# Performance work log

Hardware: AMD Instinct MI355X
Metric: run time of the kernel (lower is better)

Reference implementation:

```python
import jax, jax.numpy as jnp
import numpy as np

IMG_H = IMG_W = 640
NUM_CLASSES = 80
B = 8
NUM_ANCHORS = 76725
MAX_TOTAL = 200          # max_total_size == max_size_per_class
SCORE_TH = 0.5
IOU_TH = 0.5
K_CAND = 256             # per-class candidate pool for NMS (>= max survivors)
VARIANCES = jnp.asarray([0.1, 0.1, 0.2, 0.2], jnp.float32)


def _build_anchors(img_h, img_w):
    # RetinaNet AnchorBox: levels 3..7, 3 ratios x 3 scales, [cx, cy, w, h]
    ratios = [0.5, 1.0, 2.0]
    scales = [2.0 ** x for x in (0.0, 1.0 / 3.0, 2.0 / 3.0)]
    areas = [s * s for s in (32.0, 64.0, 128.0, 256.0, 512.0)]
    out = []
    for lvl, stride in enumerate([2 ** i for i in range(3, 8)]):
        dims = []
        for r in ratios:
            h = np.sqrt(areas[lvl] / r)
            w = areas[lvl] / h
            for s in scales:
                dims.append([w * s, h * s])
        dims = np.asarray(dims, np.float32)                      # [9,2]
        fh = int(np.ceil(img_h / stride)); fw = int(np.ceil(img_w / stride))
        rx = (np.arange(fw, dtype=np.float32) + 0.5) * stride
        ry = (np.arange(fh, dtype=np.float32) + 0.5) * stride
        cx, cy = np.meshgrid(rx, ry)
        centers = np.broadcast_to(np.stack([cx, cy], -1)[:, :, None, :], (fh, fw, 9, 2))
        d = np.broadcast_to(dims[None, None], (fh, fw, 9, 2))
        out.append(np.concatenate([centers, d], -1).reshape(-1, 4))
    return jnp.asarray(np.concatenate(out, 0))                   # [A,4]


def setup_inputs() -> dict:
    key = jax.random.key(0)
    k1, k2 = jax.random.split(key)
    box_pred = jax.random.normal(k1, (B, NUM_ANCHORS, 4), jnp.float32)
    cls_pred = jax.random.normal(k2, (B, NUM_ANCHORS, NUM_CLASSES), jnp.float32)
    anchor_boxes = _build_anchors(IMG_H, IMG_W)
    return {"box_pred": box_pred, "cls_pred": cls_pred, "anchor_boxes": anchor_boxes}


def _iou_one_vs_many(box, boxes):
    # box [4] vs boxes [K,4] in corner format
    lt = jnp.maximum(box[:2], boxes[:, :2])
    rb = jnp.minimum(box[2:], boxes[:, 2:])
    wh = jnp.maximum(rb - lt, 0.0)
    inter = wh[:, 0] * wh[:, 1]
    a1 = (box[2] - box[0]) * (box[3] - box[1])
    a2 = (boxes[:, 2] - boxes[:, 0]) * (boxes[:, 3] - boxes[:, 1])
    return inter / jnp.maximum(a1 + a2 - inter, 1e-8)


def _nms_keep(boxes, scores):
    # boxes [K,4] already sorted by descending score; greedy NMS
    eligible = scores > SCORE_TH
    idx = jnp.arange(K_CAND)

    def body(i, keep):
        iou = _iou_one_vs_many(boxes[i], boxes)
        suppress = (iou > IOU_TH) & (idx > i)
        return jnp.where(keep[i], keep & ~suppress, keep)

    keep = jax.lax.fori_loop(0, K_CAND, body, eligible)
    keep = keep & ((jnp.cumsum(keep) - 1) < MAX_TOTAL)           # max_size_per_class cap
    return keep


def _decode_and_nms(box_pred, cls_pred, anchor_boxes):
    scores_all = jax.nn.sigmoid(cls_pred)                        # [B,A,C]
    # decode: (dx,dy,dw,dh)*variances against [cx,cy,w,h] anchors
    d = box_pred * VARIANCES
    xy = d[..., :2] * anchor_boxes[None, :, 2:] + anchor_boxes[None, :, :2]
    wh = jnp.exp(d[..., 2:]) * anchor_boxes[None, :, 2:]
    boxes = jnp.concatenate([xy - 0.5 * wh, xy + 0.5 * wh], -1)  # [B,A,4] corners

    sc = jnp.swapaxes(scores_all, 1, 2)                          # [B,C,A]
    top_sc, top_idx = jax.lax.top_k(sc, K_CAND)                  # [B,C,K] sorted desc
    cand_boxes = jnp.take_along_axis(boxes[:, None], top_idx[..., None], axis=2)  # [B,C,K,4]

    keep = jax.lax.stop_gradient(jax.vmap(jax.vmap(_nms_keep))(cand_boxes, top_sc))  # [B,C,K]
    sel = jnp.where(keep, top_sc, -1.0)

    flat_sc = sel.reshape(B, -1)                                 # [B,C*K]
    flat_boxes = cand_boxes.reshape(B, -1, 4)
    flat_lbl = jnp.broadcast_to(jnp.arange(NUM_CLASSES)[None, :, None],
                                (B, NUM_CLASSES, K_CAND)).reshape(B, -1)

    fs, fi = jax.lax.top_k(flat_sc, MAX_TOTAL)                   # combine across classes
    out_boxes = jnp.take_along_axis(flat_boxes, fi[..., None], axis=1)
    out_lbl = jnp.take_along_axis(flat_lbl, fi, axis=1).astype(jnp.float32)
    valid = fs > 0.0                                             # pad invalid slots
    return (jnp.where(valid[..., None], out_boxes, 0.0),
            jnp.where(valid, fs, 0.0),
            jnp.where(valid, out_lbl, -1.0))


def reference(box_pred, cls_pred, anchor_boxes):
    return _decode_and_nms(box_pred, cls_pred, anchor_boxes)
```

## Files before the change

kernel.cpp:

```cpp
#include <hip/hip_runtime.h>
#include <math.h>
#include <stdint.h>

typedef unsigned long long u64;
typedef unsigned int u32;

#define NB 8
#define NA 76725
#define NC 80
#define KC 256
#define MAXT 200
#define CAP 2048
#define SORTN 512
#define TAU 2.0f
#define CHUNK 512
#define NCHUNK 150
#define BCAP 48
#define CSTRIDE 16

#define OFF_BUFA      0ull
#define OFF_CLASSLIST 10485760ull
#define OFF_CANDBOX   11796480ull
#define OFF_COUNTS    14417920ull

__device__ __forceinline__ void kf_proc(float4 v, int i, int a0,
                                        u64 (*bucket)[BCAP], u32* bcnt) {
  int a = a0 + i / (NC / 4);
  int c0 = (i % (NC / 4)) * 4;
  float vv[4] = {v.x, v.y, v.z, v.w};
#pragma unroll
  for (int j = 0; j < 4; j++) {
    if (vv[j] > TAU) {
      int c = c0 + j;
      u32 pos = atomicAdd(&bcnt[c], 1u);
      if (pos < BCAP)
        bucket[c][pos] = ((u64)__float_as_uint(vv[j]) << 32) | (u32)a;
    }
  }
}

__global__ __launch_bounds__(256) void kfilter(const float* __restrict__ cls,
                                               u64* __restrict__ bufA,
                                               u32* __restrict__ counts) {
  __shared__ u64 bucket[NC][BCAP];
  __shared__ u32 bcnt[NC];
  __shared__ u32 gbase[NC];
  __shared__ u32 pref[NC + 1];

  const int b = blockIdx.x / NCHUNK;
  const int ch = blockIdx.x % NCHUNK;
  const int tid = threadIdx.x;
  const int a0 = ch * CHUNK;
  const int aN = (NA - a0) < CHUNK ? (NA - a0) : CHUNK;

  for (int i = tid; i < NC; i += 256) bcnt[i] = 0;
  __syncthreads();

  const float4* p = (const float4*)(cls + ((size_t)b * NA + a0) * NC);
  const int n4 = aN * (NC / 4);
  for (int i0 = tid; i0 < n4; i0 += 1024) {
    float4 v0, v1, v2, v3;
    const bool g1 = i0 + 256 < n4, g2 = i0 + 512 < n4, g3 = i0 + 768 < n4;
    v0 = p[i0];
    if (g1) v1 = p[i0 + 256];
    if (g2) v2 = p[i0 + 512];
    if (g3) v3 = p[i0 + 768];
    kf_proc(v0, i0, a0, bucket, bcnt);
    if (g1) kf_proc(v1, i0 + 256, a0, bucket, bcnt);
    if (g2) kf_proc(v2, i0 + 512, a0, bucket, bcnt);
    if (g3) kf_proc(v3, i0 + 768, a0, bucket, bcnt);
  }
  __syncthreads();
  if (tid < NC) {
    u32 n = bcnt[tid];
    if (n > BCAP) n = BCAP;
    bcnt[tid] = n;
    gbase[tid] = atomicAdd(&counts[(b * NC + tid) * CSTRIDE], n);
  }
  __syncthreads();
  if (tid == 0) {
    u32 s = 0;
    for (int c = 0; c < NC; c++) { pref[c] = s; s += bcnt[c]; }
    pref[NC] = s;
  }
  __syncthreads();
  const int total = (int)pref[NC];
  for (int e = tid; e < total; e += 256) {
    int lo = 0, hi = NC;
    while (lo + 1 < hi) { int mid = (lo + hi) >> 1; if ((int)pref[mid] <= e) lo = mid; else hi = mid; }
    int c = lo;
    int loc = e - (int)pref[c];
    u32 gb = gbase[c] + (u32)loc;
    if (gb < CAP)
      bufA[((size_t)(b * NC + c)) * CAP + gb] = bucket[c][loc];
  }
}

__global__ __launch_bounds__(256) void kselect(
    const float* __restrict__ cls, const float* __restrict__ boxp,
    const float* __restrict__ anc, u64* __restrict__ bufA,
    const u32* __restrict__ counts, u64* __restrict__ classList,
    float4* __restrict__ candBox) {
  __shared__ u64 sbuf[CAP];
  __shared__ u32 hist[1024];
  __shared__ int sbsum[64];
  __shared__ int sT, sNsel, sExtra;
  __shared__ u64 skey[SORTN];
  __shared__ float4 sBox[KC];
  __shared__ float sAr[KC];

  const int tid = threadIdx.x;
  const int bc = blockIdx.x;
  const int b = bc / NC, c = bc % NC;
  u64* buf = bufA + (size_t)bc * CAP;

  int cnt0 = (int)counts[bc * CSTRIDE];
  if (cnt0 > CAP) cnt0 = CAP;
  int cnt = cnt0;
  if (cnt0 < KC) {
    if (tid == 0) sExtra = 0;
    __syncthreads();
    for (int a = tid; a < NA; a += 256) {
      float x = cls[((size_t)b * NA + a) * NC + c];
      if (x > 0.0f && !(x > TAU)) {
        int pos = cnt0 + atomicAdd(&sExtra, 1);
        if (pos < CAP) buf[pos] = ((u64)__float_as_uint(x) << 32) | (u32)a;
      }
    }
    __syncthreads();
    cnt = cnt0 + sExtra;
  }
  if (cnt > CAP) cnt = CAP;

  for (int i = tid; i < 1024; i += 256) hist[i] = 0;
  if (tid == 0) sNsel = 0;
  for (int e = tid; e < cnt; e += 256) sbuf[e] = buf[e];
  __syncthreads();

  for (int e = tid; e < cnt; e += 256) {
    float f = __uint_as_float((u32)(sbuf[e] >> 32));
    int bin = (int)(f * 170.0f);
    bin = bin < 0 ? 0 : (bin > 1023 ? 1023 : bin);
    atomicAdd(&hist[bin], 1u);
  }
  __syncthreads();
  if (tid < 64) {
    int s = 0;
    for (int i = 0; i < 16; i++) s += (int)hist[tid * 16 + i];
    sbsum[tid] = s;
  }
  __syncthreads();
  if (tid == 0) {
    int acc = 0, sb = 63;
    while (sb >= 0 && acc + sbsum[sb] < KC) { acc += sbsum[sb]; sb--; }
    int T = 0;
    if (sb >= 0) {
      int bin = sb * 16 + 15;
      while (bin > sb * 16 && acc + (int)hist[bin] < KC) {
        acc += (int)hist[bin];
        bin--;
      }
      T = bin;
    }
    sT = T;
  }
  __syncthreads();
  const int T = sT;

  for (int e = tid; e < cnt; e += 256) {
    u64 k = sbuf[e];
    float f = __uint_as_float((u32)(k >> 32));
    int bin = (int)(f * 170.0f);
    bin = bin < 0 ? 0 : (bin > 1023 ? 1023 : bin);
    if (bin >= T) {
      float sc = 1.0f / (1.0f + expf(-f));
      u32 a = (u32)k;
      int pos = atomicAdd(&sNsel, 1);
      if (pos < SORTN)
        skey[pos] = ((u64)__float_as_uint(sc) << 32) | (0xFFFFFFFFu - a);
    }
  }
  __syncthreads();
  int nsel = sNsel;
  if (nsel > SORTN) nsel = SORTN;
  for (int i = tid; i < SORTN; i += 256)
    if (i >= nsel) skey[i] = 0;
  __syncthreads();

  for (int k = 2; k <= SORTN; k <<= 1) {
    for (int j = k >> 1; j > 0; j >>= 1) {
      int i = ((tid & ~(j - 1)) << 1) | (tid & (j - 1));
      int ixj = i | j;
      u64 x = skey[i], y = skey[ixj];
      bool desc = ((i & k) == 0);
      if (desc ? (x < y) : (x > y)) { skey[i] = y; skey[ixj] = x; }
      __syncthreads();
    }
  }

  {
    u64 k = skey[tid];
    u32 a = 0xFFFFFFFFu - (u32)k;
    if (k == 0ull || a >= NA) a = 0;
    float4 p = ((const float4*)boxp)[(size_t)b * NA + a];
    float4 an = ((const float4*)anc)[a];
    float dx = __fmul_rn(p.x, 0.1f), dy = __fmul_rn(p.y, 0.1f);
    float dw = __fmul_rn(p.z, 0.2f), dh = __fmul_rn(p.w, 0.2f);
    float cx = __fadd_rn(__fmul_rn(dx, an.z), an.x);
    float cy = __fadd_rn(__fmul_rn(dy, an.w), an.y);
    float w = __fmul_rn(expf(dw), an.z);
    float h = __fmul_rn(expf(dh), an.w);
    float4 bx;
    bx.x = __fsub_rn(cx, __fmul_rn(0.5f, w));
    bx.y = __fsub_rn(cy, __fmul_rn(0.5f, h));
    bx.z = __fadd_rn(cx, __fmul_rn(0.5f, w));
    bx.w = __fadd_rn(cy, __fmul_rn(0.5f, h));
    sBox[tid] = bx;
    sAr[tid] = __fmul_rn(__fsub_rn(bx.z, bx.x), __fsub_rn(bx.w, bx.y));
    candBox[(size_t)bc * KC + tid] = bx;
  }
  __syncthreads();

  if (tid < 64) {
    const int ln = tid;
    float x1[4], y1[4], x2[4], y2[4], ar[4];
    int keep = 0;
#pragma unroll
    for (int s = 0; s < 4; s++) {
      int j = s * 64 + ln;
      float4 bj = sBox[j];
      x1[s] = bj.x; y1[s] = bj.y; x2[s] = bj.z; y2[s] = bj.w;
      ar[s] = sAr[j];
      if (skey[j] != 0ull) keep |= (1 << s);
    }
    for (int i = 0; i < KC; i++) {
      float4 bi = sBox[i];
      float ai = sAr[i];
      int sup = 0;
#pragma unroll
      for (int s = 0; s < 4; s++) {
        int j = s * 64 + ln;
        float lx = fmaxf(bi.x, x1[s]), ly = fmaxf(bi.y, y1[s]);
        float rx = fminf(bi.z, x2[s]), ry = fminf(bi.w, y2[s]);
        float wx = fmaxf(__fsub_rn(rx, lx), 0.0f);
        float wy = fmaxf(__fsub_rn(ry, ly), 0.0f);
        float inter = __fmul_rn(wx, wy);
        float uni = fmaxf(__fsub_rn(__fadd_rn(ai, ar[s]), inter), 1e-8f);
        float iou = __fdiv_rn(inter, uni);
        if (j > i && iou > 0.5f) sup |= (1 << s);
      }
      int ki = __shfl(keep, i & 63, 64);
      if ((ki >> (i >> 6)) & 1) keep &= ~sup;
    }
    u64 m[4];
#pragma unroll
    for (int s = 0; s < 4; s++) m[s] = __ballot((keep >> s) & 1);
    int tot = 0;
#pragma unroll
    for (int s = 0; s < 4; s++) tot += __popcll(m[s]);
    int keptTotal = tot < MAXT ? tot : MAXT;
    u64 lmask = (1ull << ln) - 1ull;
    int base = 0;
#pragma unroll
    for (int s = 0; s < 4; s++) {
      int j = s * 64 + ln;
      int cum = base + (int)__popcll(m[s] & lmask);
      if (((keep >> s) & 1) && cum < MAXT) {
        u64 hi = skey[j] >> 32;
        classList[(size_t)bc * KC + cum] =
            (hi << 32) | (u64)(0xFFFFFFFFu - (u32)(c * KC + j));
      }
      base += (int)__popcll(m[s]);
    }
    for (int t2 = ln; t2 < KC; t2 += 64)
      if (t2 >= keptTotal) classList[(size_t)bc * KC + t2] = 0;
  }
}

__device__ __forceinline__ u64 shfl64(u64 v, int src) {
  int lo = __shfl((int)(u32)v, src, 64);
  int hi = __shfl((int)(v >> 32), src, 64);
  return ((u64)(u32)hi << 32) | (u32)lo;
}
__device__ __forceinline__ u64 shflxor64(u64 v, int mask) {
  int lo = __shfl_xor((int)(u32)v, mask, 64);
  int hi = __shfl_xor((int)(v >> 32), mask, 64);
  return ((u64)(u32)hi << 32) | (u32)lo;
}
#define CSWAP(a, b) { if ((a) < (b)) { u64 _t = (a); (a) = (b); (b) = _t; } }

__device__ __forceinline__ void wave_merge(u64 acc[4], const u64 cur[4], int ln) {
  u64 t0 = shfl64(cur[3], 63 - ln);
  u64 t1 = shfl64(cur[2], 63 - ln);
  u64 t2 = shfl64(cur[1], 63 - ln);
  u64 t3 = shfl64(cur[0], 63 - ln);
  acc[0] = acc[0] > t0 ? acc[0] : t0;
  acc[1] = acc[1] > t1 ? acc[1] : t1;
  acc[2] = acc[2] > t2 ? acc[2] : t2;
  acc[3] = acc[3] > t3 ? acc[3] : t3;
  CSWAP(acc[0], acc[2]); CSWAP(acc[1], acc[3]);
  CSWAP(acc[0], acc[1]); CSWAP(acc[2], acc[3]);
#pragma unroll
  for (int s = 32; s >= 1; s >>= 1) {
#pragma unroll
    for (int k = 0; k < 4; k++) {
      u64 o = shflxor64(acc[k], s);
      u64 mx = acc[k] > o ? acc[k] : o;
      u64 mn = acc[k] < o ? acc[k] : o;
      acc[k] = ((ln & s) == 0) ? mx : mn;
    }
  }
}

__global__ __launch_bounds__(256) void kmerge(const u64* __restrict__ classList,
                                              const float4* __restrict__ candBox,
                                              float* __restrict__ out) {
  __shared__ u64 lds[4 * KC];
  const int tid = threadIdx.x, b = blockIdx.x;
  const int w = tid >> 6, ln = tid & 63;
  const u64* base = classList + ((size_t)b * NC + w * 20) * KC;
  u64 acc[4];
#pragma unroll
  for (int k = 0; k < 4; k++) acc[k] = base[k * 64 + ln];
  for (int m = 1; m < 20; m++) {
    u64 cur[4];
#pragma unroll
    for (int k = 0; k < 4; k++) cur[k] = base[(size_t)m * KC + k * 64 + ln];
    wave_merge(acc, cur, ln);
  }
#pragma unroll
  for (int k = 0; k < 4; k++) lds[w * KC + k * 64 + ln] = acc[k];
  __syncthreads();
  if (w == 0) {
    for (int m = 1; m < 4; m++) {
      u64 cur[4];
#pragma unroll
      for (int k = 0; k < 4; k++) cur[k] = lds[m * KC + k * 64 + ln];
      wave_merge(acc, cur, ln);
    }
#pragma unroll
    for (int k = 0; k < 4; k++) lds[k * 64 + ln] = acc[k];
  }
  __syncthreads();
  if (tid < MAXT) {
    u64 k = lds[tid];
    float4 bx = make_float4(0.f, 0.f, 0.f, 0.f);
    float sc = 0.0f, lb = -1.0f;
    if (k != 0ull) {
      sc = __uint_as_float((u32)(k >> 32));
      u32 flat = 0xFFFFFFFFu - (u32)k;
      int cc = (int)(flat >> 8), kk = (int)(flat & 255u);
      bx = candBox[((size_t)b * NC + cc) * KC + kk];
      lb = (float)cc;
    }
    float* ob = out + ((size_t)b * MAXT + tid) * 4;
    ob[0] = bx.x; ob[1] = bx.y; ob[2] = bx.z; ob[3] = bx.w;
    out[NB * MAXT * 4 + b * MAXT + tid] = sc;
    out[NB * MAXT * 4 + NB * MAXT + b * MAXT + tid] = lb;
  }
}

extern "C" void kernel_launch(void* const* d_in, const int* in_sizes, int n_in,
                              void* d_out, int out_size, void* d_ws,
                              size_t ws_size, hipStream_t stream) {
  const float* boxp = (const float*)d_in[0];
  const float* cls = (const float*)d_in[1];
  const float* anc = (const float*)d_in[2];
  char* ws = (char*)d_ws;
  u64* bufA = (u64*)(ws + OFF_BUFA);
  u64* classList = (u64*)(ws + OFF_CLASSLIST);
  float4* candBox = (float4*)(ws + OFF_CANDBOX);
  u32* counts = (u32*)(ws + OFF_COUNTS);

  hipMemsetAsync(counts, 0, NB * NC * CSTRIDE * sizeof(u32), stream);
  kfilter<<<NB * NCHUNK, 256, 0, stream>>>(cls, bufA, counts);
  kselect<<<NB * NC, 256, 0, stream>>>(cls, boxp, anc, bufA, counts, classList,
                                       candBox);
  kmerge<<<NB, 256, 0, stream>>>(classList, candBox, (float*)d_out);
}
```

Baseline: 410.5 us.

## Replace bitonic sort with rank sort and precompute NMS IoU bitmask matrix

Measured after the change: 390.2 us. 1.05x faster.

```diff
diff --git a/kernel.cpp b/kernel.cpp
--- a/kernel.cpp
+++ b/kernel.cpp
@@ -11,7 +11,7 @@
 #define KC 256
 #define MAXT 200
 #define CAP 2048
-#define SORTN 512
+#define SELCAP 768
 #define TAU 2.0f
 #define CHUNK 512
 #define NCHUNK 150
@@ -58,17 +58,17 @@
 
   const float4* p = (const float4*)(cls + ((size_t)b * NA + a0) * NC);
   const int n4 = aN * (NC / 4);
-  for (int i0 = tid; i0 < n4; i0 += 1024) {
-    float4 v0, v1, v2, v3;
-    const bool g1 = i0 + 256 < n4, g2 = i0 + 512 < n4, g3 = i0 + 768 < n4;
-    v0 = p[i0];
-    if (g1) v1 = p[i0 + 256];
-    if (g2) v2 = p[i0 + 512];
-    if (g3) v3 = p[i0 + 768];
-    kf_proc(v0, i0, a0, bucket, bcnt);
-    if (g1) kf_proc(v1, i0 + 256, a0, bucket, bcnt);
-    if (g2) kf_proc(v2, i0 + 512, a0, bucket, bcnt);
-    if (g3) kf_proc(v3, i0 + 768, a0, bucket, bcnt);
+  for (int i0 = tid; i0 < n4; i0 += 2048) {
+    float4 v[8];
+    bool g[8];
+#pragma unroll
+    for (int u = 0; u < 8; u++) {
+      g[u] = (i0 + u * 256) < n4;
+      if (g[u]) v[u] = p[i0 + u * 256];
+    }
+#pragma unroll
+    for (int u = 0; u < 8; u++)
+      if (g[u]) kf_proc(v[u], i0 + u * 256, a0, bucket, bcnt);
   }
   __syncthreads();
   if (tid < NC) {
@@ -103,11 +103,12 @@
     float4* __restrict__ candBox) {
   __shared__ u64 sbuf[CAP];
   __shared__ u32 hist[1024];
-  __shared__ int sbsum[64];
-  __shared__ int sT, sNsel, sExtra;
-  __shared__ u64 skey[SORTN];
+  __shared__ u64 sel[SELCAP];
+  __shared__ u64 skey[KC];
+  __shared__ u64 scolT[4][KC];
   __shared__ float4 sBox[KC];
   __shared__ float sAr[KC];
+  __shared__ int sNsel, sExtra, sSb;
 
   const int tid = threadIdx.x;
   const int bc = blockIdx.x;
@@ -134,6 +135,7 @@
 
   for (int i = tid; i < 1024; i += 256) hist[i] = 0;
   if (tid == 0) sNsel = 0;
+  skey[tid] = 0;
   for (int e = tid; e < cnt; e += 256) sbuf[e] = buf[e];
   __syncthreads();
 
@@ -144,59 +146,48 @@
     atomicAdd(&hist[bin], 1u);
   }
   __syncthreads();
+
   if (tid < 64) {
     int s = 0;
+#pragma unroll
     for (int i = 0; i < 16; i++) s += (int)hist[tid * 16 + i];
-    sbsum[tid] = s;
-  }
-  __syncthreads();
-  if (tid == 0) {
-    int acc = 0, sb = 63;
-    while (sb >= 0 && acc + sbsum[sb] < KC) { acc += sbsum[sb]; sb--; }
-    int T = 0;
-    if (sb >= 0) {
-      int bin = sb * 16 + 15;
-      while (bin > sb * 16 && acc + (int)hist[bin] < KC) {
-        acc += (int)hist[bin];
-        bin--;
-      }
-      T = bin;
-    }
-    sT = T;
-  }
-  __syncthreads();
-  const int T = sT;
+    int suf = s;
+#pragma unroll
+    for (int d = 1; d < 64; d <<= 1) {
+      int t = __shfl_down(suf, d, 64);
+      if (tid + d < 64) suf += t;
+    }
+    u64 mask = __ballot(suf >= KC);
+    int sb = mask ? (63 - __clzll((long long)mask)) : 0;
+    if (tid == 0) sSb = sb;
+  }
+  __syncthreads();
+  const int sb = sSb;
 
   for (int e = tid; e < cnt; e += 256) {
     u64 k = sbuf[e];
     float f = __uint_as_float((u32)(k >> 32));
     int bin = (int)(f * 170.0f);
     bin = bin < 0 ? 0 : (bin > 1023 ? 1023 : bin);
-    if (bin >= T) {
+    if ((bin >> 4) >= sb) {
       float sc = 1.0f / (1.0f + expf(-f));
       u32 a = (u32)k;
       int pos = atomicAdd(&sNsel, 1);
-      if (pos < SORTN)
-        skey[pos] = ((u64)__float_as_uint(sc) << 32) | (0xFFFFFFFFu - a);
+      if (pos < SELCAP)
+        sel[pos] = ((u64)__float_as_uint(sc) << 32) | (0xFFFFFFFFu - a);
     }
   }
   __syncthreads();
   int nsel = sNsel;
-  if (nsel > SORTN) nsel = SORTN;
-  for (int i = tid; i < SORTN; i += 256)
-    if (i >= nsel) skey[i] = 0;
-  __syncthreads();
-
-  for (int k = 2; k <= SORTN; k <<= 1) {
-    for (int j = k >> 1; j > 0; j >>= 1) {
-      int i = ((tid & ~(j - 1)) << 1) | (tid & (j - 1));
-      int ixj = i | j;
-      u64 x = skey[i], y = skey[ixj];
-      bool desc = ((i & k) == 0);
-      if (desc ? (x < y) : (x > y)) { skey[i] = y; skey[ixj] = x; }
-      __syncthreads();
-    }
-  }
+  if (nsel > SELCAP) nsel = SELCAP;
+
+  for (int e = tid; e < nsel; e += 256) {
+    u64 k = sel[e];
+    int r = 0;
+    for (int q = 0; q < nsel; q++) r += (sel[q] > k) ? 1 : 0;
+    if (r < KC) skey[r] = k;
+  }
+  __syncthreads();
 
   {
     u64 k = skey[tid];
@@ -221,36 +212,50 @@
   }
   __syncthreads();
 
+  {
+    const int j = tid;
+    float4 bj = sBox[j];
+    float aj = sAr[j];
+    u64 cw[4] = {0ull, 0ull, 0ull, 0ull};
+    for (int i = 0; i < j; i++) {
+      float4 bi = sBox[i];
+      float ai = sAr[i];
+      float lx = fmaxf(bi.x, bj.x), ly = fmaxf(bi.y, bj.y);
+      float rx = fminf(bi.z, bj.z), ry = fminf(bi.w, bj.w);
+      float wx = fmaxf(__fsub_rn(rx, lx), 0.0f);
+      float wy = fmaxf(__fsub_rn(ry, ly), 0.0f);
+      float inter = __fmul_rn(wx, wy);
+      float uni = fmaxf(__fsub_rn(__fadd_rn(ai, aj), inter), 1e-8f);
+      float iou = __fdiv_rn(inter, uni);
+      if (iou > 0.5f) cw[i >> 6] |= (1ull << (i & 63));
+    }
+#pragma unroll
+    for (int w = 0; w < 4; w++) scolT[w][j] = cw[w];
+  }
+  __syncthreads();
+
   if (tid < 64) {
     const int ln = tid;
-    float x1[4], y1[4], x2[4], y2[4], ar[4];
+    u64 C[4][4];
+#pragma unroll
+    for (int s = 0; s < 4; s++)
+#pragma unroll
+      for (int w = 0; w < 4; w++) C[s][w] = scolT[w][s * 64 + ln];
     int keep = 0;
 #pragma unroll
-    for (int s = 0; s < 4; s++) {
-      int j = s * 64 + ln;
-      float4 bj = sBox[j];
-      x1[s] = bj.x; y1[s] = bj.y; x2[s] = bj.z; y2[s] = bj.w;
-      ar[s] = sAr[j];
-      if (skey[j] != 0ull) keep |= (1 << s);
-    }
-    for (int i = 0; i < KC; i++) {
-      float4 bi = sBox[i];
-      float ai = sAr[i];
-      int sup = 0;
-#pragma unroll
-      for (int s = 0; s < 4; s++) {
-        int j = s * 64 + ln;
-        float lx = fmaxf(bi.x, x1[s]), ly = fmaxf(bi.y, y1[s]);
-        float rx = fminf(bi.z, x2[s]), ry = fminf(bi.w, y2[s]);
-        float wx = fmaxf(__fsub_rn(rx, lx), 0.0f);
-        float wy = fmaxf(__fsub_rn(ry, ly), 0.0f);
-        float inter = __fmul_rn(wx, wy);
-        float uni = fmaxf(__fsub_rn(__fadd_rn(ai, ar[s]), inter), 1e-8f);
-        float iou = __fdiv_rn(inter, uni);
-        if (j > i && iou > 0.5f) sup |= (1 << s);
+    for (int s = 0; s < 4; s++)
+      if (skey[s * 64 + ln] != 0ull) keep |= (1 << s);
+#pragma unroll
+    for (int w = 0; w < 4; w++) {
+      u64 c0 = C[0][w], c1 = C[1][w], c2 = C[2][w], c3 = C[3][w];
+      for (int t = 0; t < 64; t++) {
+        int kt = __shfl(keep, t, 64);
+        if ((kt >> w) & 1) {
+          int sup = (int)((c0 >> t) & 1) | ((int)((c1 >> t) & 1) << 1) |
+                    ((int)((c2 >> t) & 1) << 2) | ((int)((c3 >> t) & 1) << 3);
+          keep &= ~sup;
+        }
       }
-      int ki = __shfl(keep, i & 63, 64);
-      if ((ki >> (i >> 6)) & 1) keep &= ~sup;
     }
     u64 m[4];
 #pragma unroll
```
